# Kernel tuning notes

Measured on AMD Instinct MI355X. Metric: run time of the kernel, lower is better.

Reference implementation:

```python
import jax, jax.numpy as jnp
import numpy as np

N, E = 100000, 640000
D_IN = 128          # in_channels
D_OUT = 128         # out_channels (= heads * per-head C)
H, C = 2, 64        # heads, out_channels // 2
MSG = 128           # msg_dim
TD = 128            # time_enc.out_channels
EDGE_DIM = MSG + TD # 256


def setup_inputs() -> dict:
    key = jax.random.key(0)
    ks = jax.random.split(key, 16)
    s_in = 1.0 / np.sqrt(D_IN)
    s_e = 1.0 / np.sqrt(EDGE_DIM)
    return {
        "x": jax.random.normal(ks[0], (N, D_IN), jnp.float32),
        "last_update": jax.random.uniform(ks[1], (N,), jnp.float32, 0.0, 1000.0),
        "t": jax.random.uniform(ks[2], (E,), jnp.float32, 0.0, 1000.0),
        "msg": jax.random.normal(ks[3], (E, MSG), jnp.float32),
        "w_time": jax.random.normal(ks[4], (TD,), jnp.float32),      # Linear(1, TD) weight
        "b_time": jax.random.normal(ks[5], (TD,), jnp.float32) * 0.1,
        "W_q": jax.random.normal(ks[6], (D_IN, H * C), jnp.float32) * s_in,
        "b_q": jnp.zeros((H * C,), jnp.float32),
        "W_k": jax.random.normal(ks[7], (D_IN, H * C), jnp.float32) * s_in,
        "b_k": jnp.zeros((H * C,), jnp.float32),
        "W_v": jax.random.normal(ks[8], (D_IN, H * C), jnp.float32) * s_in,
        "b_v": jnp.zeros((H * C,), jnp.float32),
        "W_e": jax.random.normal(ks[9], (EDGE_DIM, H * C), jnp.float32) * s_e,  # lin_edge, no bias
        "W_skip": jax.random.normal(ks[10], (D_IN, H * C), jnp.float32) * s_in,
        "b_skip": jnp.zeros((H * C,), jnp.float32),
        "edge_index": jax.random.randint(ks[11], (2, E), 0, N, jnp.int64),
    }


def _forward(x, last_update, t, msg, w_time, b_time, W_q, b_q, W_k, b_k,
             W_v, b_v, W_e, W_skip, b_skip, edge_index):
    src, dst = edge_index[0], edge_index[1]
    n = x.shape[0]
    # time encoding of relative time: cos(Linear(1 -> TD))
    rel_t = last_update[src] - t                               # [E]
    rel_t_enc = jnp.cos(rel_t[:, None] * w_time + b_time)      # [E, TD]
    edge_attr = jnp.concatenate([msg, rel_t_enc], axis=-1)     # [E, EDGE_DIM]

    q = (x @ W_q + b_q).reshape(n, H, C)[dst]                  # [E, H, C]
    k = (x @ W_k + b_k)[src].reshape(-1, H, C)                 # [E, H, C]
    v = (x @ W_v + b_v)[src].reshape(-1, H, C)                 # [E, H, C]
    e = (edge_attr @ W_e).reshape(-1, H, C)                    # [E, H, C]
    k = k + e

    alpha = jnp.einsum('ehc,ehc->eh', q, k) / jnp.sqrt(jnp.float32(C))  # [E, H]
    # scatter-softmax over destination nodes
    m = jax.ops.segment_max(alpha, dst, num_segments=n)        # [n, H]
    ea = jnp.exp(alpha - m[dst])
    denom = jax.ops.segment_sum(ea, dst, num_segments=n)       # [n, H]
    attn = ea / (denom[dst] + 1e-16)                           # [E, H]

    out_e = (v + e) * attn[:, :, None]                         # [E, H, C]
    out = jax.ops.segment_sum(out_e, dst, num_segments=n)      # [n, H, C]
    out = out.reshape(n, H * C)
    return out + x @ W_skip + b_skip                           # root skip (beta=False)


def reference(x, last_update, t, msg, w_time, b_time, W_q, b_q, W_k, b_k,
              W_v, b_v, W_e, W_skip, b_skip, edge_index):
    return _forward(x, last_update, t, msg, w_time, b_time, W_q, b_q, W_k, b_k,
                    W_v, b_v, W_e, W_skip, b_skip, edge_index)
```

## Files before the change

### kernel.cpp

```cpp
#include <hip/hip_runtime.h>
#include <hip/hip_bf16.h>
#include <math.h>

#define NN   100000
#define NE   640000
#define DIN  128
#define DO   128
#define ED   256
#define MSGD 128
#define NBLK 391

typedef __attribute__((ext_vector_type(8))) short s16x8;
typedef __attribute__((ext_vector_type(4))) float f32x4;
typedef __attribute__((ext_vector_type(4))) unsigned short u16x4;
typedef __attribute__((ext_vector_type(8))) unsigned short u16x8;

__device__ __forceinline__ unsigned short f2bs(float f) {
    __hip_bfloat16 h = __float2bfloat16(f);
    return __builtin_bit_cast(unsigned short, h);
}
__device__ __forceinline__ float bs2f(unsigned short u) {
    return __uint_as_float(((unsigned int)u) << 16);
}
__device__ __forceinline__ float fast_cos(float x) {
    float rev = x * 0.15915494309189535f;
    rev = rev - rintf(rev);
    return __builtin_amdgcn_cosf(rev);
}

__global__ __launch_bounds__(256) void convert_kernel(
    const float* __restrict__ We,
    const float* __restrict__ Wq, const float* __restrict__ Wk,
    const float* __restrict__ Wv, const float* __restrict__ Ws,
    unsigned short* __restrict__ WeT,
    unsigned short* __restrict__ WqT, unsigned short* __restrict__ WkT,
    unsigned short* __restrict__ WvT, unsigned short* __restrict__ WsT)
{
    const int T0  = ED * DO;
    const int TOT = T0 + 4 * DIN * DO;
    int i = blockIdx.x * 256 + threadIdx.x;
    if (i >= TOT) return;
    if (i < T0) {
        int n = i >> 8, k = i & 255;
        WeT[i] = f2bs(We[(size_t)k * DO + n]);
    } else {
        int j = i - T0; int m = j >> 14; int r = j & 16383;
        int n = r >> 7, k = r & 127;
        const float* W = (m == 0) ? Wq : (m == 1) ? Wk : (m == 2) ? Wv : Ws;
        unsigned short* WD = (m == 0) ? WqT : (m == 1) ? WkT : (m == 2) ? WvT : WsT;
        WD[r] = f2bs(W[(size_t)k * DO + n]);
    }
}

__global__ __launch_bounds__(256) void node_proj_kernel(
    const float* __restrict__ x,
    const unsigned short* __restrict__ WqT, const float* __restrict__ bq,
    const unsigned short* __restrict__ WkT, const float* __restrict__ bk,
    const unsigned short* __restrict__ WvT, const float* __restrict__ bv,
    const unsigned short* __restrict__ WsT, const float* __restrict__ bs,
    unsigned short* __restrict__ Qb, unsigned short* __restrict__ Kb,
    unsigned short* __restrict__ Vb, float* __restrict__ SKIP)
{
    __shared__ unsigned short xt[64 * 136];
    const int tid = threadIdx.x;
    const int n0  = blockIdx.x * 64;

    #pragma unroll
    for (int i = 0; i < 8; ++i) {
        int q = i * 256 + tid; int row = q >> 5, c4 = q & 31;
        int gn = n0 + row; if (gn > NN - 1) gn = NN - 1;
        float4 v = ((const float4*)(x + (size_t)gn * DIN))[c4];
        u16x4 b; b.x = f2bs(v.x); b.y = f2bs(v.y); b.z = f2bs(v.z); b.w = f2bs(v.w);
        *(u16x4*)(xt + row * 136 + c4 * 4) = b;
    }
    __syncthreads();

    const int lane = tid & 63, w = tid >> 6;
    const int l15 = lane & 15, quad = lane >> 4;
    const unsigned short* arow = xt + (w * 16 + l15) * 136 + quad * 8;

    const unsigned short* WT[4] = {WqT, WkT, WvT, WsT};
    const float*          BI[4] = {bq, bk, bv, bs};

    #pragma unroll
    for (int m = 0; m < 4; ++m) {
        f32x4 acc[8];
        #pragma unroll
        for (int j = 0; j < 8; ++j) { float b = BI[m][j * 16 + l15]; acc[j] = {b, b, b, b}; }
        const unsigned short* Wm = WT[m];
        #pragma unroll
        for (int ks = 0; ks < 4; ++ks) {
            s16x8 a = *(const s16x8*)(arow + ks * 32);
            #pragma unroll
            for (int j = 0; j < 8; ++j) {
                s16x8 bf = *(const s16x8*)(Wm + (j * 16 + l15) * DIN + ks * 32 + quad * 8);
                acc[j] = __builtin_amdgcn_mfma_f32_16x16x32_bf16(a, bf, acc[j], 0, 0, 0);
            }
        }
        #pragma unroll
        for (int j = 0; j < 8; ++j) {
            int col = j * 16 + l15;
            #pragma unroll
            for (int r = 0; r < 4; ++r) {
                int node = n0 + w * 16 + quad * 4 + r;
                if (node < NN) {
                    float v = acc[j][r];
                    if (m == 0)      Qb[(size_t)node * DO + col] = f2bs(v);
                    else if (m == 1) Kb[(size_t)node * DO + col] = f2bs(v);
                    else if (m == 2) Vb[(size_t)node * DO + col] = f2bs(v);
                    else             SKIP[(size_t)node * DO + col] = v;
                }
            }
        }
    }
}

__global__ __launch_bounds__(256) void hist_kernel(
    const int* __restrict__ dstI, int* __restrict__ counts)
{
    int e = blockIdx.x * 256 + threadIdx.x;
    if (e < NE) atomicAdd(&counts[dstI[e]], 1);
}

__global__ __launch_bounds__(256) void scan1_kernel(
    const int* __restrict__ counts, int* __restrict__ bsum)
{
    __shared__ int s[256];
    int t = threadIdx.x; int i = blockIdx.x * 256 + t;
    s[t] = (i < NN) ? counts[i] : 0;
    __syncthreads();
    #pragma unroll
    for (int off = 128; off; off >>= 1) {
        if (t < off) s[t] += s[t + off];
        __syncthreads();
    }
    if (t == 0) bsum[blockIdx.x] = s[0];
}

__global__ __launch_bounds__(512) void scan2_kernel(int* __restrict__ bsum)
{
    __shared__ int s[512];
    int t = threadIdx.x;
    int v = (t < NBLK) ? bsum[t] : 0;
    s[t] = v; __syncthreads();
    for (int off = 1; off < 512; off <<= 1) {
        int add = (t >= off) ? s[t - off] : 0;
        __syncthreads();
        s[t] += add;
        __syncthreads();
    }
    if (t < NBLK) bsum[t] = s[t] - v;
}

__global__ __launch_bounds__(256) void scan3_kernel(
    const int* __restrict__ counts, const int* __restrict__ bsum,
    int* __restrict__ rowptr)
{
    __shared__ int s[256];
    int t = threadIdx.x; int i = blockIdx.x * 256 + t;
    int v = (i < NN) ? counts[i] : 0;
    s[t] = v; __syncthreads();
    for (int off = 1; off < 256; off <<= 1) {
        int add = (t >= off) ? s[t - off] : 0;
        __syncthreads();
        s[t] += add;
        __syncthreads();
    }
    if (i < NN) rowptr[i] = bsum[blockIdx.x] + s[t] - v;
    if (i == 0) rowptr[NN] = NE;
}

__global__ __launch_bounds__(256) void scatter_kernel(
    const int* __restrict__ dstI, const int* __restrict__ rowptr,
    int* __restrict__ cursor, int* __restrict__ rank)
{
    int e = blockIdx.x * 256 + threadIdx.x;
    if (e < NE) {
        int d = dstI[e];
        int pos = rowptr[d] + atomicAdd(&cursor[d], 1);
        rank[e] = pos;
    }
}

__global__ __launch_bounds__(256) void edge_kernel(
    const float* __restrict__ last_update, const float* __restrict__ tarr,
    const float* __restrict__ msg,
    const float* __restrict__ w_time, const float* __restrict__ b_time,
    const unsigned short* __restrict__ WeT,
    const int* __restrict__ srcI, const int* __restrict__ dstI,
    const int* __restrict__ rank,
    const unsigned short* __restrict__ Qb, const unsigned short* __restrict__ Kb,
    const unsigned short* __restrict__ Vb,
    unsigned short* __restrict__ VE, float* __restrict__ EA)
{
    __shared__ char  smem[32 * 528];
    __shared__ int   ssrc[32], sdst[32], srk[32];
    __shared__ float srel[32];
    const int tid = threadIdx.x;
    const int e0  = blockIdx.x * 32;

    if (tid < 32) {
        int s = srcI[e0 + tid], d = dstI[e0 + tid];
        ssrc[tid] = s; sdst[tid] = d; srk[tid] = rank[e0 + tid];
        srel[tid] = last_update[s] - tarr[e0 + tid];
    }
    __syncthreads();

    const int ql   = tid & 3;
    const int task = tid >> 2;
    const int te   = task >> 1;
    const int th   = task & 1;
    const int tc0  = th * 64 + ql * 16;
    const int ts = ssrc[te], td = sdst[te];
    const unsigned short* qp = Qb + (size_t)td * DO + tc0;
    const unsigned short* kp = Kb + (size_t)ts * DO + tc0;
    const unsigned short* vp = Vb + (size_t)ts * DO + tc0;
    u16x8 q0 = *(const u16x8*)qp,  q1 = *(const u16x8*)(qp + 8);
    u16x8 k0 = *(const u16x8*)kp,  k1 = *(const u16x8*)(kp + 8);
    u16x8 v0 = *(const u16x8*)vp,  v1 = *(const u16x8*)(vp + 8);

    unsigned short* at = (unsigned short*)smem;
    const float4* msg4 = (const float4*)msg;
    #pragma unroll
    for (int i = 0; i < 4; ++i) {
        int q = i * 256 + tid; int e = q >> 5, c4 = q & 31;
        float4 m4 = msg4[(size_t)(e0 + e) * 32 + c4];
        u16x4 b; b.x = f2bs(m4.x); b.y = f2bs(m4.y); b.z = f2bs(m4.z); b.w = f2bs(m4.w);
        *(u16x4*)(at + e * 264 + c4 * 4) = b;
    }
    #pragma unroll
    for (int i = 0; i < 16; ++i) {
        int q = i * 256 + tid; int e = q >> 7, j = q & 127;
        float v = fast_cos(srel[e] * w_time[j] + b_time[j]);
        at[e * 264 + MSGD + j] = f2bs(v);
    }
    __syncthreads();

    const int lane = tid & 63, w = tid >> 6;
    const int l15 = lane & 15, quad = lane >> 4;
    const int rh = (w & 1) * 16;
    const int chh = (w >> 1) * 64;

    f32x4 acc[4];
    #pragma unroll
    for (int j = 0; j < 4; ++j) acc[j] = {0.f, 0.f, 0.f, 0.f};
    const unsigned short* arow = at + (rh + l15) * 264 + quad * 8;
    #pragma unroll
    for (int ks = 0; ks < 8; ++ks) {
        s16x8 a = *(const s16x8*)(arow + ks * 32);
        #pragma unroll
        for (int j = 0; j < 4; ++j) {
            s16x8 b = *(const s16x8*)(WeT + (size_t)(chh + j * 16 + l15) * ED + ks * 32 + quad * 8);
            acc[j] = __builtin_amdgcn_mfma_f32_16x16x32_bf16(a, b, acc[j], 0, 0, 0);
        }
    }
    __syncthreads();

    float* eld = (float*)smem;
    #pragma unroll
    for (int j = 0; j < 4; ++j) {
        #pragma unroll
        for (int r = 0; r < 4; ++r)
            eld[(rh + quad * 4 + r) * 132 + chh + j * 16 + l15] = acc[j][r];
    }
    __syncthreads();

    const f32x4* ep4 = (const f32x4*)(eld + te * 132 + tc0);
    float p = 0.f;
    u16x8 o0, o1;
    #pragma unroll
    for (int i = 0; i < 8; ++i) {
        float ev = ep4[i >> 2][i & 3];
        p += bs2f((unsigned short)q0[i]) * (bs2f((unsigned short)k0[i]) + ev);
        o0[i] = (unsigned short)f2bs(bs2f((unsigned short)v0[i]) + ev);
    }
    #pragma unroll
    for (int i = 0; i < 8; ++i) {
        float ev = ep4[2 + (i >> 2)][i & 3];
        p += bs2f((unsigned short)q1[i]) * (bs2f((unsigned short)k1[i]) + ev);
        o1[i] = (unsigned short)f2bs(bs2f((unsigned short)v1[i]) + ev);
    }
    p += __shfl_xor(p, 1, 64);
    p += __shfl_xor(p, 2, 64);
    float ea = __expf(p * 0.125f);
    int pos = srk[te];
    unsigned short* vep = VE + (size_t)pos * DO + tc0;
    *(u16x8*)vep       = o0;
    *(u16x8*)(vep + 8) = o1;
    if (ql == 0) EA[(size_t)pos * 2 + th] = ea;
}

__global__ __launch_bounds__(256) void agg_kernel(
    const int* __restrict__ rowptr,
    const float* __restrict__ EA, const unsigned short* __restrict__ VE,
    const float* __restrict__ SKIP, float* __restrict__ out)
{
    int wid  = (blockIdx.x * 256 + threadIdx.x) >> 6;
    int lane = threadIdx.x & 63;
    if (wid >= NN) return;
    int beg = rowptr[wid], end = rowptr[wid + 1];
    float a0 = 0.f, a1 = 0.f, den = 0.f;
    int j = beg;
    for (; j + 1 < end; j += 2) {
        float2 eaA = ((const float2*)EA)[j];
        float2 eaB = ((const float2*)EA)[j + 1];
        unsigned int pvA = ((const unsigned int*)(VE + (size_t)j * DO))[lane];
        unsigned int pvB = ((const unsigned int*)(VE + (size_t)(j + 1) * DO))[lane];
        float eA = (lane < 32) ? eaA.x : eaA.y;
        float eB = (lane < 32) ? eaB.x : eaB.y;
        den += eA + eB;
        a0 += eA * bs2f((unsigned short)(pvA & 0xffffu))
            + eB * bs2f((unsigned short)(pvB & 0xffffu));
        a1 += eA * bs2f((unsigned short)(pvA >> 16))
            + eB * bs2f((unsigned short)(pvB >> 16));
    }
    if (j < end) {
        float2 ea = ((const float2*)EA)[j];
        unsigned int pv = ((const unsigned int*)(VE + (size_t)j * DO))[lane];
        float eh = (lane < 32) ? ea.x : ea.y;
        den += eh;
        a0 += eh * bs2f((unsigned short)(pv & 0xffffu));
        a1 += eh * bs2f((unsigned short)(pv >> 16));
    }
    float inv = 1.0f / (den + 1e-16f);
    float2 sk = ((const float2*)SKIP)[(size_t)wid * 64 + lane];
    float2 o;
    o.x = a0 * inv + sk.x;
    o.y = a1 * inv + sk.y;
    ((float2*)out)[(size_t)wid * 64 + lane] = o;
}

extern "C" void kernel_launch(void* const* d_in, const int* in_sizes, int n_in,
                              void* d_out, int out_size, void* d_ws, size_t ws_size,
                              hipStream_t stream) {
    const float* x           = (const float*)d_in[0];
    const float* last_update = (const float*)d_in[1];
    const float* tarr        = (const float*)d_in[2];
    const float* msg         = (const float*)d_in[3];
    const float* w_time      = (const float*)d_in[4];
    const float* b_time      = (const float*)d_in[5];
    const float* Wq          = (const float*)d_in[6];
    const float* bq          = (const float*)d_in[7];
    const float* Wk          = (const float*)d_in[8];
    const float* bk          = (const float*)d_in[9];
    const float* Wv          = (const float*)d_in[10];
    const float* bv          = (const float*)d_in[11];
    const float* We          = (const float*)d_in[12];
    const float* Ws          = (const float*)d_in[13];
    const float* bs          = (const float*)d_in[14];
    const int*   ei          = (const int*)d_in[15];
    const int*   srcI = ei;
    const int*   dstI = ei + NE;

    float* out = (float*)d_out;
    char*  ws  = (char*)d_ws;
    unsigned short* Qb   = (unsigned short*)(ws);
    unsigned short* Kb   = (unsigned short*)(ws + 25600000);
    unsigned short* Vb   = (unsigned short*)(ws + 51200000);
    unsigned short* WeT  = (unsigned short*)(ws + 76800000);
    unsigned short* WqT  = (unsigned short*)(ws + 76865536);
    unsigned short* WkT  = (unsigned short*)(ws + 76898304);
    unsigned short* WvT  = (unsigned short*)(ws + 76931072);
    unsigned short* WsT  = (unsigned short*)(ws + 76963840);
    float*          SKIP = (float*)(ws + 76996608);
    unsigned short* VE   = (unsigned short*)(ws + 128196608);
    float*          EA   = (float*)(ws + 292036608);
    int*            rank = (int*)(ws + 297156608);
    int*            counts = (int*)(ws + 299716608);
    int*            cursor = (int*)(ws + 300116608);
    int*            rowptr = (int*)(ws + 300516608);
    int*            bsum   = (int*)(ws + 300916624);

    hipMemsetAsync(counts, 0, 800000, stream);

    convert_kernel<<<384, 256, 0, stream>>>(
        We, Wq, Wk, Wv, Ws, WeT, WqT, WkT, WvT, WsT);

    node_proj_kernel<<<(NN + 63) / 64, 256, 0, stream>>>(
        x, WqT, bq, WkT, bk, WvT, bv, WsT, bs, Qb, Kb, Vb, SKIP);

    hist_kernel<<<(NE + 255) / 256, 256, 0, stream>>>(dstI, counts);
    scan1_kernel<<<NBLK, 256, 0, stream>>>(counts, bsum);
    scan2_kernel<<<1, 512, 0, stream>>>(bsum);
    scan3_kernel<<<NBLK, 256, 0, stream>>>(counts, bsum, rowptr);
    scatter_kernel<<<(NE + 255) / 256, 256, 0, stream>>>(dstI, rowptr, cursor, rank);

    edge_kernel<<<NE / 32, 256, 0, stream>>>(
        last_update, tarr, msg, w_time, b_time, WeT, srcI, dstI, rank,
        Qb, Kb, Vb, VE, EA);

    agg_kernel<<<(NN * 64 + 255) / 256, 256, 0, stream>>>(
        rowptr, EA, VE, SKIP, out);
}
```

Measured before the change: 1.005 ms.

## Process edges in CSR order, fuse histogram, write skip directly to output

The scatter kernel now writes a packed per-edge record (src, dst, original id, relative time) in destination-sorted order. The edge kernel walks edges in that order, so its VE/EA writes are contiguous and the Q rows for a destination are reused across neighbouring edges, at the cost of gathering msg rows through a permutation. The edge kernel now handles 64 edges per block with two MFMA accumulators per wave, sharing the weight fragments across both. The histogram is folded into the weight conversion kernel, and node projection uses swapped MFMA operands for vectorized stores, writing the skip term straight into the output buffer so the SKIP workspace and its round trip go away.

```diff
diff --git a/kernel.cpp b/kernel.cpp
--- a/kernel.cpp
+++ b/kernel.cpp
@@ -28,28 +28,31 @@
     return __builtin_amdgcn_cosf(rev);
 }
 
-__global__ __launch_bounds__(256) void convert_kernel(
+__global__ __launch_bounds__(256) void convert_hist_kernel(
     const float* __restrict__ We,
     const float* __restrict__ Wq, const float* __restrict__ Wk,
     const float* __restrict__ Wv, const float* __restrict__ Ws,
     unsigned short* __restrict__ WeT,
     unsigned short* __restrict__ WqT, unsigned short* __restrict__ WkT,
-    unsigned short* __restrict__ WvT, unsigned short* __restrict__ WsT)
+    unsigned short* __restrict__ WvT, unsigned short* __restrict__ WsT,
+    const int* __restrict__ dstI, int* __restrict__ counts)
 {
     const int T0  = ED * DO;
     const int TOT = T0 + 4 * DIN * DO;
     int i = blockIdx.x * 256 + threadIdx.x;
-    if (i >= TOT) return;
-    if (i < T0) {
-        int n = i >> 8, k = i & 255;
-        WeT[i] = f2bs(We[(size_t)k * DO + n]);
-    } else {
-        int j = i - T0; int m = j >> 14; int r = j & 16383;
-        int n = r >> 7, k = r & 127;
-        const float* W = (m == 0) ? Wq : (m == 1) ? Wk : (m == 2) ? Wv : Ws;
-        unsigned short* WD = (m == 0) ? WqT : (m == 1) ? WkT : (m == 2) ? WvT : WsT;
-        WD[r] = f2bs(W[(size_t)k * DO + n]);
-    }
+    if (i < TOT) {
+        if (i < T0) {
+            int n = i >> 8, k = i & 255;
+            WeT[i] = f2bs(We[(size_t)k * DO + n]);
+        } else {
+            int j = i - T0; int m = j >> 14; int r = j & 16383;
+            int n = r >> 7, k = r & 127;
+            const float* W = (m == 0) ? Wq : (m == 1) ? Wk : (m == 2) ? Wv : Ws;
+            unsigned short* WD = (m == 0) ? WqT : (m == 1) ? WkT : (m == 2) ? WvT : WsT;
+            WD[r] = f2bs(W[(size_t)k * DO + n]);
+        }
+    }
+    if (i < NE) atomicAdd(&counts[dstI[i]], 1);
 }
 
 __global__ __launch_bounds__(256) void node_proj_kernel(
@@ -59,7 +62,7 @@
     const unsigned short* __restrict__ WvT, const float* __restrict__ bv,
     const unsigned short* __restrict__ WsT, const float* __restrict__ bs,
     unsigned short* __restrict__ Qb, unsigned short* __restrict__ Kb,
-    unsigned short* __restrict__ Vb, float* __restrict__ SKIP)
+    unsigned short* __restrict__ Vb, float* __restrict__ out)
 {
     __shared__ unsigned short xt[64 * 136];
     const int tid = threadIdx.x;
@@ -77,7 +80,8 @@
 
     const int lane = tid & 63, w = tid >> 6;
     const int l15 = lane & 15, quad = lane >> 4;
-    const unsigned short* arow = xt + (w * 16 + l15) * 136 + quad * 8;
+    const unsigned short* brow = xt + (w * 16 + l15) * 136 + quad * 8;
+    const int node = n0 + w * 16 + l15;
 
     const unsigned short* WT[4] = {WqT, WkT, WvT, WsT};
     const float*          BI[4] = {bq, bk, bv, bs};
@@ -86,40 +90,34 @@
     for (int m = 0; m < 4; ++m) {
         f32x4 acc[8];
         #pragma unroll
-        for (int j = 0; j < 8; ++j) { float b = BI[m][j * 16 + l15]; acc[j] = {b, b, b, b}; }
+        for (int j = 0; j < 8; ++j)
+            acc[j] = *(const f32x4*)(BI[m] + j * 16 + quad * 4);
         const unsigned short* Wm = WT[m];
         #pragma unroll
         for (int ks = 0; ks < 4; ++ks) {
-            s16x8 a = *(const s16x8*)(arow + ks * 32);
+            s16x8 bx = *(const s16x8*)(brow + ks * 32);
             #pragma unroll
             for (int j = 0; j < 8; ++j) {
-                s16x8 bf = *(const s16x8*)(Wm + (j * 16 + l15) * DIN + ks * 32 + quad * 8);
-                acc[j] = __builtin_amdgcn_mfma_f32_16x16x32_bf16(a, bf, acc[j], 0, 0, 0);
+                s16x8 aw = *(const s16x8*)(Wm + (size_t)(j * 16 + l15) * DIN + ks * 32 + quad * 8);
+                acc[j] = __builtin_amdgcn_mfma_f32_16x16x32_bf16(aw, bx, acc[j], 0, 0, 0);
             }
         }
-        #pragma unroll
-        for (int j = 0; j < 8; ++j) {
-            int col = j * 16 + l15;
+        if (node < NN) {
             #pragma unroll
-            for (int r = 0; r < 4; ++r) {
-                int node = n0 + w * 16 + quad * 4 + r;
-                if (node < NN) {
-                    float v = acc[j][r];
-                    if (m == 0)      Qb[(size_t)node * DO + col] = f2bs(v);
-                    else if (m == 1) Kb[(size_t)node * DO + col] = f2bs(v);
-                    else if (m == 2) Vb[(size_t)node * DO + col] = f2bs(v);
-                    else             SKIP[(size_t)node * DO + col] = v;
+            for (int j = 0; j < 8; ++j) {
+                int c0 = j * 16 + quad * 4;
+                if (m == 3) {
+                    *(f32x4*)(out + (size_t)node * DO + c0) = acc[j];
+                } else {
+                    u16x4 pk;
+                    pk.x = f2bs(acc[j][0]); pk.y = f2bs(acc[j][1]);
+                    pk.z = f2bs(acc[j][2]); pk.w = f2bs(acc[j][3]);
+                    unsigned short* Dst = (m == 0) ? Qb : (m == 1) ? Kb : Vb;
+                    *(u16x4*)(Dst + (size_t)node * DO + c0) = pk;
                 }
             }
         }
     }
-}
-
-__global__ __launch_bounds__(256) void hist_kernel(
-    const int* __restrict__ dstI, int* __restrict__ counts)
-{
-    int e = blockIdx.x * 256 + threadIdx.x;
-    if (e < NE) atomicAdd(&counts[dstI[e]], 1);
 }
 
 __global__ __launch_bounds__(256) void scan1_kernel(
@@ -171,65 +169,74 @@
 }
 
 __global__ __launch_bounds__(256) void scatter_kernel(
-    const int* __restrict__ dstI, const int* __restrict__ rowptr,
-    int* __restrict__ cursor, int* __restrict__ rank)
+    const int* __restrict__ srcI, const int* __restrict__ dstI,
+    const float* __restrict__ last_update, const float* __restrict__ tarr,
+    const int* __restrict__ rowptr, int* __restrict__ cursor,
+    int4* __restrict__ meta)
 {
     int e = blockIdx.x * 256 + threadIdx.x;
     if (e < NE) {
-        int d = dstI[e];
+        int d = dstI[e], s = srcI[e];
         int pos = rowptr[d] + atomicAdd(&cursor[d], 1);
-        rank[e] = pos;
+        float rel = last_update[s] - tarr[e];
+        meta[pos] = make_int4(s, d, e, __float_as_int(rel));
     }
 }
 
 __global__ __launch_bounds__(256) void edge_kernel(
-    const float* __restrict__ last_update, const float* __restrict__ tarr,
     const float* __restrict__ msg,
     const float* __restrict__ w_time, const float* __restrict__ b_time,
     const unsigned short* __restrict__ WeT,
-    const int* __restrict__ srcI, const int* __restrict__ dstI,
-    const int* __restrict__ rank,
+    const int4* __restrict__ meta,
     const unsigned short* __restrict__ Qb, const unsigned short* __restrict__ Kb,
     const unsigned short* __restrict__ Vb,
     unsigned short* __restrict__ VE, float* __restrict__ EA)
 {
-    __shared__ char  smem[32 * 528];
-    __shared__ int   ssrc[32], sdst[32], srk[32];
-    __shared__ float srel[32];
+    __shared__ char  smem[64 * 528];
+    __shared__ int   ssrc[64], sdst[64], sperm[64];
+    __shared__ float srel[64];
     const int tid = threadIdx.x;
-    const int e0  = blockIdx.x * 32;
-
-    if (tid < 32) {
-        int s = srcI[e0 + tid], d = dstI[e0 + tid];
-        ssrc[tid] = s; sdst[tid] = d; srk[tid] = rank[e0 + tid];
-        srel[tid] = last_update[s] - tarr[e0 + tid];
-    }
-    __syncthreads();
-
-    const int ql   = tid & 3;
-    const int task = tid >> 2;
-    const int te   = task >> 1;
-    const int th   = task & 1;
-    const int tc0  = th * 64 + ql * 16;
-    const int ts = ssrc[te], td = sdst[te];
-    const unsigned short* qp = Qb + (size_t)td * DO + tc0;
-    const unsigned short* kp = Kb + (size_t)ts * DO + tc0;
-    const unsigned short* vp = Vb + (size_t)ts * DO + tc0;
-    u16x8 q0 = *(const u16x8*)qp,  q1 = *(const u16x8*)(qp + 8);
-    u16x8 k0 = *(const u16x8*)kp,  k1 = *(const u16x8*)(kp + 8);
-    u16x8 v0 = *(const u16x8*)vp,  v1 = *(const u16x8*)(vp + 8);
+    const int e0  = blockIdx.x * 64;
+
+    if (tid < 64) {
+        int4 m = meta[e0 + tid];
+        ssrc[tid]  = m.x;
+        sdst[tid]  = m.y;
+        sperm[tid] = m.z;
+        srel[tid]  = __int_as_float(m.w);
+    }
+    __syncthreads();
+
+    const int ql  = tid & 3;
+    const int th  = (tid >> 2) & 1;
+    const int te  = tid >> 3;
+    const int tc0 = th * 64 + ql * 16;
+    const int sA = ssrc[te],      dA = sdst[te];
+    const int sB = ssrc[te + 32], dB = sdst[te + 32];
+    const unsigned short* qpA = Qb + (size_t)dA * DO + tc0;
+    const unsigned short* kpA = Kb + (size_t)sA * DO + tc0;
+    const unsigned short* vpA = Vb + (size_t)sA * DO + tc0;
+    const unsigned short* qpB = Qb + (size_t)dB * DO + tc0;
+    const unsigned short* kpB = Kb + (size_t)sB * DO + tc0;
+    const unsigned short* vpB = Vb + (size_t)sB * DO + tc0;
+    u16x8 qA0 = *(const u16x8*)qpA, qA1 = *(const u16x8*)(qpA + 8);
+    u16x8 kA0 = *(const u16x8*)kpA, kA1 = *(const u16x8*)(kpA + 8);
+    u16x8 vA0 = *(const u16x8*)vpA, vA1 = *(const u16x8*)(vpA + 8);
+    u16x8 qB0 = *(const u16x8*)qpB, qB1 = *(const u16x8*)(qpB + 8);
+    u16x8 kB0 = *(const u16x8*)kpB, kB1 = *(const u16x8*)(kpB + 8);
+    u16x8 vB0 = *(const u16x8*)vpB, vB1 = *(const u16x8*)(vpB + 8);
 
     unsigned short* at = (unsigned short*)smem;
     const float4* msg4 = (const float4*)msg;
     #pragma unroll
-    for (int i = 0; i < 4; ++i) {
+    for (int i = 0; i < 8; ++i) {
         int q = i * 256 + tid; int e = q >> 5, c4 = q & 31;
-        float4 m4 = msg4[(size_t)(e0 + e) * 32 + c4];
+        float4 m4 = msg4[(size_t)sperm[e] * 32 + c4];
         u16x4 b; b.x = f2bs(m4.x); b.y = f2bs(m4.y); b.z = f2bs(m4.z); b.w = f2bs(m4.w);
         *(u16x4*)(at + e * 264 + c4 * 4) = b;
     }
     #pragma unroll
-    for (int i = 0; i < 16; ++i) {
+    for (int i = 0; i < 32; ++i) {
         int q = i * 256 + tid; int e = q >> 7, j = q & 127;
         float v = fast_cos(srel[e] * w_time[j] + b_time[j]);
         at[e * 264 + MSGD + j] = f2bs(v);
@@ -238,20 +245,23 @@
 
     const int lane = tid & 63, w = tid >> 6;
     const int l15 = lane & 15, quad = lane >> 4;
-    const int rh = (w & 1) * 16;
-    const int chh = (w >> 1) * 64;
-
-    f32x4 acc[4];
-    #pragma unroll
-    for (int j = 0; j < 4; ++j) acc[j] = {0.f, 0.f, 0.f, 0.f};
-    const unsigned short* arow = at + (rh + l15) * 264 + quad * 8;
+    const int chh = (w & 1) * 64;
+    const int g0  = (w >> 1) * 2, g1 = g0 + 1;
+
+    f32x4 acc0[4], acc1[4];
+    #pragma unroll
+    for (int j = 0; j < 4; ++j) { acc0[j] = {0.f,0.f,0.f,0.f}; acc1[j] = {0.f,0.f,0.f,0.f}; }
+    const unsigned short* b0row = at + (g0 * 16 + l15) * 264 + quad * 8;
+    const unsigned short* b1row = at + (g1 * 16 + l15) * 264 + quad * 8;
     #pragma unroll
     for (int ks = 0; ks < 8; ++ks) {
-        s16x8 a = *(const s16x8*)(arow + ks * 32);
+        s16x8 b0 = *(const s16x8*)(b0row + ks * 32);
+        s16x8 b1 = *(const s16x8*)(b1row + ks * 32);
         #pragma unroll
         for (int j = 0; j < 4; ++j) {
-            s16x8 b = *(const s16x8*)(WeT + (size_t)(chh + j * 16 + l15) * ED + ks * 32 + quad * 8);
-            acc[j] = __builtin_amdgcn_mfma_f32_16x16x32_bf16(a, b, acc[j], 0, 0, 0);
+            s16x8 a = *(const s16x8*)(WeT + (size_t)(chh + j * 16 + l15) * ED + ks * 32 + quad * 8);
+            acc0[j] = __builtin_amdgcn_mfma_f32_16x16x32_bf16(a, b0, acc0[j], 0, 0, 0);
+            acc1[j] = __builtin_amdgcn_mfma_f32_16x16x32_bf16(a, b1, acc1[j], 0, 0, 0);
         }
     }
     __syncthreads();
@@ -259,41 +269,65 @@
     float* eld = (float*)smem;
     #pragma unroll
     for (int j = 0; j < 4; ++j) {
-        #pragma unroll
-        for (int r = 0; r < 4; ++r)
-            eld[(rh + quad * 4 + r) * 132 + chh + j * 16 + l15] = acc[j][r];
-    }
-    __syncthreads();
-
-    const f32x4* ep4 = (const f32x4*)(eld + te * 132 + tc0);
-    float p = 0.f;
-    u16x8 o0, o1;
-    #pragma unroll
-    for (int i = 0; i < 8; ++i) {
-        float ev = ep4[i >> 2][i & 3];
-        p += bs2f((unsigned short)q0[i]) * (bs2f((unsigned short)k0[i]) + ev);
-        o0[i] = (unsigned short)f2bs(bs2f((unsigned short)v0[i]) + ev);
-    }
-    #pragma unroll
-    for (int i = 0; i < 8; ++i) {
-        float ev = ep4[2 + (i >> 2)][i & 3];
-        p += bs2f((unsigned short)q1[i]) * (bs2f((unsigned short)k1[i]) + ev);
-        o1[i] = (unsigned short)f2bs(bs2f((unsigned short)v1[i]) + ev);
-    }
-    p += __shfl_xor(p, 1, 64);
-    p += __shfl_xor(p, 2, 64);
-    float ea = __expf(p * 0.125f);
-    int pos = srk[te];
-    unsigned short* vep = VE + (size_t)pos * DO + tc0;
-    *(u16x8*)vep       = o0;
-    *(u16x8*)(vep + 8) = o1;
-    if (ql == 0) EA[(size_t)pos * 2 + th] = ea;
+        *(f32x4*)(eld + (g0 * 16 + l15) * 132 + chh + j * 16 + quad * 4) = acc0[j];
+        *(f32x4*)(eld + (g1 * 16 + l15) * 132 + chh + j * 16 + quad * 4) = acc1[j];
+    }
+    __syncthreads();
+
+    {
+        const f32x4* ep4 = (const f32x4*)(eld + te * 132 + tc0);
+        float p = 0.f;
+        u16x8 o0, o1;
+        #pragma unroll
+        for (int i = 0; i < 8; ++i) {
+            float ev = ep4[i >> 2][i & 3];
+            p += bs2f((unsigned short)qA0[i]) * (bs2f((unsigned short)kA0[i]) + ev);
+            o0[i] = (unsigned short)f2bs(bs2f((unsigned short)vA0[i]) + ev);
+        }
+        #pragma unroll
+        for (int i = 0; i < 8; ++i) {
+            float ev = ep4[2 + (i >> 2)][i & 3];
+            p += bs2f((unsigned short)qA1[i]) * (bs2f((unsigned short)kA1[i]) + ev);
+            o1[i] = (unsigned short)f2bs(bs2f((unsigned short)vA1[i]) + ev);
+        }
+        p += __shfl_xor(p, 1, 64);
+        p += __shfl_xor(p, 2, 64);
+        float ea = __expf(p * 0.125f);
+        unsigned short* vep = VE + (size_t)(e0 + te) * DO + tc0;
+        *(u16x8*)vep       = o0;
+        *(u16x8*)(vep + 8) = o1;
+        if (ql == 0) EA[(size_t)(e0 + te) * 2 + th] = ea;
+    }
+    {
+        const f32x4* ep4 = (const f32x4*)(eld + (te + 32) * 132 + tc0);
+        float p = 0.f;
+        u16x8 o0, o1;
+        #pragma unroll
+        for (int i = 0; i < 8; ++i) {
+            float ev = ep4[i >> 2][i & 3];
+            p += bs2f((unsigned short)qB0[i]) * (bs2f((unsigned short)kB0[i]) + ev);
+            o0[i] = (unsigned short)f2bs(bs2f((unsigned short)vB0[i]) + ev);
+        }
+        #pragma unroll
+        for (int i = 0; i < 8; ++i) {
+            float ev = ep4[2 + (i >> 2)][i & 3];
+            p += bs2f((unsigned short)qB1[i]) * (bs2f((unsigned short)kB1[i]) + ev);
+            o1[i] = (unsigned short)f2bs(bs2f((unsigned short)vB1[i]) + ev);
+        }
+        p += __shfl_xor(p, 1, 64);
+        p += __shfl_xor(p, 2, 64);
+        float ea = __expf(p * 0.125f);
+        unsigned short* vep = VE + (size_t)(e0 + te + 32) * DO + tc0;
+        *(u16x8*)vep       = o0;
+        *(u16x8*)(vep + 8) = o1;
+        if (ql == 0) EA[(size_t)(e0 + te + 32) * 2 + th] = ea;
+    }
 }
 
 __global__ __launch_bounds__(256) void agg_kernel(
     const int* __restrict__ rowptr,
     const float* __restrict__ EA, const unsigned short* __restrict__ VE,
-    const float* __restrict__ SKIP, float* __restrict__ out)
+    float* __restrict__ out)
 {
     int wid  = (blockIdx.x * 256 + threadIdx.x) >> 6;
     int lane = threadIdx.x & 63;
@@ -323,7 +357,7 @@
         a1 += eh * bs2f((unsigned short)(pv >> 16));
     }
     float inv = 1.0f / (den + 1e-16f);
-    float2 sk = ((const float2*)SKIP)[(size_t)wid * 64 + lane];
+    float2 sk = ((const float2*)out)[(size_t)wid * 64 + lane];
     float2 o;
     o.x = a0 * inv + sk.x;
     o.y = a1 * inv + sk.y;
@@ -362,33 +396,31 @@
     unsigned short* WkT  = (unsigned short*)(ws + 76898304);
     unsigned short* WvT  = (unsigned short*)(ws + 76931072);
     unsigned short* WsT  = (unsigned short*)(ws + 76963840);
-    float*          SKIP = (float*)(ws + 76996608);
-    unsigned short* VE   = (unsigned short*)(ws + 128196608);
-    float*          EA   = (float*)(ws + 292036608);
-    int*            rank = (int*)(ws + 297156608);
-    int*            counts = (int*)(ws + 299716608);
-    int*            cursor = (int*)(ws + 300116608);
-    int*            rowptr = (int*)(ws + 300516608);
-    int*            bsum   = (int*)(ws + 300916624);
+    unsigned short* VE   = (unsigned short*)(ws + 76996608);
+    float*          EA   = (float*)(ws + 240836608);
+    int4*           meta = (int4*)(ws + 245956608);
+    int*            rowptr = (int*)(ws + 256196608);
+    int*            counts = (int*)(ws + 256596624);
+    int*            cursor = (int*)(ws + 256996624);
+    int*            bsum   = (int*)(ws + 257396624);
 
     hipMemsetAsync(counts, 0, 800000, stream);
 
-    convert_kernel<<<384, 256, 0, stream>>>(
-        We, Wq, Wk, Wv, Ws, WeT, WqT, WkT, WvT, WsT);
+    convert_hist_kernel<<<(NE + 255) / 256, 256, 0, stream>>>(
+        We, Wq, Wk, Wv, Ws, WeT, WqT, WkT, WvT, WsT, dstI, counts);
 
     node_proj_kernel<<<(NN + 63) / 64, 256, 0, stream>>>(
-        x, WqT, bq, WkT, bk, WvT, bv, WsT, bs, Qb, Kb, Vb, SKIP);
-
-    hist_kernel<<<(NE + 255) / 256, 256, 0, stream>>>(dstI, counts);
+        x, WqT, bq, WkT, bk, WvT, bv, WsT, bs, Qb, Kb, Vb, out);
+
     scan1_kernel<<<NBLK, 256, 0, stream>>>(counts, bsum);
     scan2_kernel<<<1, 512, 0, stream>>>(bsum);
     scan3_kernel<<<NBLK, 256, 0, stream>>>(counts, bsum, rowptr);
-    scatter_kernel<<<(NE + 255) / 256, 256, 0, stream>>>(dstI, rowptr, cursor, rank);
-
-    edge_kernel<<<NE / 32, 256, 0, stream>>>(
-        last_update, tarr, msg, w_time, b_time, WeT, srcI, dstI, rank,
-        Qb, Kb, Vb, VE, EA);
+    scatter_kernel<<<(NE + 255) / 256, 256, 0, stream>>>(
+        srcI, dstI, last_update, tarr, rowptr, cursor, meta);
+
+    edge_kernel<<<NE / 64, 256, 0, stream>>>(
+        msg, w_time, b_time, WeT, meta, Qb, Kb, Vb, VE, EA);
 
     agg_kernel<<<(NN * 64 + 255) / 256, 256, 0, stream>>>(
-        rowptr, EA, VE, SKIP, out);
-}
+        rowptr, EA, VE, out);
+}
```

Measured after the change: 941.2 us. 6.4% less time.
